# Optimization experiments

Hardware: AMD Instinct MI355X
Metric: run time of the kernel (lower is better)

Reference implementation:

```python
import jax, jax.numpy as jnp
import numpy as np

B, C, H, W = 16, 32, 32, 2048


def setup_inputs() -> dict:
    key = jax.random.key(0)
    ks = jax.random.split(key, 7)
    s = 1.0 / np.sqrt(C * H)  # torch conv2d default init scale (fan_in = C*H*1)
    x = jax.random.normal(ks[0], (B, C, H, W), dtype=jnp.float32)
    wq = jax.random.uniform(ks[1], (C, C, H), jnp.float32, -s, s)
    bq = jax.random.uniform(ks[2], (C,), jnp.float32, -s, s)
    wk = jax.random.uniform(ks[3], (C, C, H), jnp.float32, -s, s)
    bk = jax.random.uniform(ks[4], (C,), jnp.float32, -s, s)
    wv = jax.random.uniform(ks[5], (C, C, H), jnp.float32, -s, s)
    bv = jax.random.uniform(ks[6], (C,), jnp.float32, -s, s)
    return {"x": x, "wq": wq, "bq": bq, "wk": wk, "bk": bk, "wv": wv, "bv": bv}


def _proj(x, w, b):
    # Conv2d kernel (H,1) with no padding == contract over (in_channels, H).
    # x: [B,C,H,W], w: [Cout,Cin,H] -> [B,Cout,W]
    return jnp.einsum('bihw,oih->bow', x, w) + b[None, :, None]


def reference(x, wq, bq, wk, bk, wv, bv):
    q = _proj(x, wq, bq)            # [B,C,W]
    k = _proj(x, wk, bk)            # [B,C,W]
    v = _proj(x, wv, bv)            # [B,C,W]
    # query.permute(0,2,1) @ key -> [B,W,W]; NOTE: unscaled, as in source.
    scores = jnp.einsum('bcw,bcv->bwv', q, k)
    attn = jax.nn.softmax(scores, axis=-1)
    # value @ attention^T -> [B,C,W]
    out = jnp.einsum('bcv,bwv->bcw', v, attn)
    # bilinear upsample (1,W)->(H,W), align_corners=False: width is identity,
    # height replicates the single row -> pure broadcast. Then residual add.
    return out[:, :, None, :] + x
```

## Files before the change

kernel.cpp:

```cpp
#include <hip/hip_runtime.h>
#include <hip/hip_bf16.h>

typedef __bf16 bf16x8 __attribute__((ext_vector_type(8)));
typedef float  f32x4  __attribute__((ext_vector_type(4)));
typedef float  f32x16 __attribute__((ext_vector_type(16)));

#define NB 16
#define NC 32
#define NH 32
#define NW 2048
#define NK (NC*NH)
#define LOG2E 1.4426950408889634f
#define KP 40

static __device__ __forceinline__ unsigned int pk2(float a, float b) {
    union { __bf16 h[2]; unsigned int u; } z;
    z.h[0] = (__bf16)a; z.h[1] = (__bf16)b;
    return z.u;
}

__global__ __launch_bounds__(256) void wprep_kernel(
    const float* __restrict__ wq, const float* __restrict__ wk,
    const float* __restrict__ wv, __bf16* __restrict__ wb)
{
    const int i = blockIdx.x * 256 + threadIdx.x;
    const float* srcs[3] = { wq, wk, wv };
    float4 v = *(const float4*)(srcs[i >> 13] + (size_t)(i & 8191) * 4);
    const float sc = (i >> 13) == 0 ? LOG2E : 1.0f;
    union { __bf16 h[4]; unsigned long long u; } z;
    z.h[0] = (__bf16)(v.x * sc); z.h[1] = (__bf16)(v.y * sc);
    z.h[2] = (__bf16)(v.z * sc); z.h[3] = (__bf16)(v.w * sc);
    *(unsigned long long*)(wb + (size_t)i * 4) = z.u;
}

__global__ __launch_bounds__(384) void proj_kernel(
    const float* __restrict__ x, const __bf16* __restrict__ wb,
    const float* __restrict__ bq, const float* __restrict__ bk,
    const float* __restrict__ bv,
    __bf16* __restrict__ qT, __bf16* __restrict__ kT, __bf16* __restrict__ V)
{
    const int b    = blockIdx.x >> 6;
    const int wt   = blockIdx.x & 63;
    const int nt   = threadIdx.x >> 6;
    const int lane = threadIdx.x & 63;
    const int g    = lane >> 4;
    const int lr   = lane & 15;
    const int w0   = wt * 32;

    __shared__ __bf16 tile[2][32][KP];

    const float* xb = x + (size_t)b * NK * NW;

    const int skr = threadIdx.x >> 3;
    const int swc = (threadIdx.x & 7) * 4;
    const bool stager = (threadIdx.x < 256);
    const float* xs = xb + w0 + swc;

    const __bf16* wrow = wb + (size_t)(nt >> 1) * 32768
                            + (size_t)((nt & 1) * 16 + lr) * NK;

    f32x4 acc0 = {0.f,0.f,0.f,0.f}, acc1 = {0.f,0.f,0.f,0.f};

    f32x4 xv;
    if (stager) {
        xv = *(const f32x4*)(xs + (size_t)skr * NW);
        __bf16* wp = &tile[0][swc][skr];
        wp[0*KP] = (__bf16)xv[0]; wp[1*KP] = (__bf16)xv[1];
        wp[2*KP] = (__bf16)xv[2]; wp[3*KP] = (__bf16)xv[3];
    }
    bf16x8 Bcur = *(const bf16x8*)(wrow + g*8);
    __syncthreads();

    for (int s = 0; s < 32; ++s) {
        const int cur = s & 1;
        f32x4 xn;
        if (s < 31 && stager)
            xn = *(const f32x4*)(xs + (size_t)((s+1)*32 + skr) * NW);
        bf16x8 Bnext;
        if (s < 31)
            Bnext = *(const bf16x8*)(wrow + (s+1)*32 + g*8);

        const bf16x8 af0 = *(const bf16x8*)&tile[cur][lr][g*8];
        const bf16x8 af1 = *(const bf16x8*)&tile[cur][16 + lr][g*8];
        acc0 = __builtin_amdgcn_mfma_f32_16x16x32_bf16(af0, Bcur, acc0, 0, 0, 0);
        acc1 = __builtin_amdgcn_mfma_f32_16x16x32_bf16(af1, Bcur, acc1, 0, 0, 0);

        if (s < 31 && stager) {
            __bf16* wp = &tile[cur ^ 1][swc][skr];
            wp[0*KP] = (__bf16)xn[0]; wp[1*KP] = (__bf16)xn[1];
            wp[2*KP] = (__bf16)xn[2]; wp[3*KP] = (__bf16)xn[3];
        }
        Bcur = Bnext;
        __syncthreads();
    }

    const int pid = nt >> 1;
    const int o   = (nt & 1) * 16 + lr;
    const float* biases[3] = { bq, bk, bv };
    float bb = biases[pid][o];
    if (pid == 0) bb *= LOG2E;

    if (pid < 2) {
        __bf16* dst = (pid ? kT : qT) + (size_t)b * NW * NC;
        #pragma unroll
        for (int r = 0; r < 4; ++r) {
            dst[(size_t)(w0 +      g*4 + r) * NC + o] = (__bf16)(acc0[r] + bb);
            dst[(size_t)(w0 + 16 + g*4 + r) * NC + o] = (__bf16)(acc1[r] + bb);
        }
    } else {
        __bf16* dst = V + ((size_t)b * NC + o) * NW + w0;
        union { __bf16 h[4]; unsigned long long u; } z0, z1;
        #pragma unroll
        for (int r = 0; r < 4; ++r) {
            z0.h[r] = (__bf16)(acc0[r] + bb);
            z1.h[r] = (__bf16)(acc1[r] + bb);
        }
        *(unsigned long long*)(dst +      g*4) = z0.u;
        *(unsigned long long*)(dst + 16 + g*4) = z1.u;
    }
}

__global__ __launch_bounds__(256) void attn_kernel(
    const float* __restrict__ x,
    const __bf16* __restrict__ qT, const __bf16* __restrict__ kT,
    const __bf16* __restrict__ V,
    float* __restrict__ out)
{
    const int b    = blockIdx.x >> 6;
    const int wt   = blockIdx.x & 63;
    const int w0   = wt * 32;
    const int wave = threadIdx.x >> 6;
    const int lane = threadIdx.x & 63;
    const int wl = lane & 31, hi = lane >> 5;
    const int swl = (wl & 0x13) | ((wl & 4) << 1) | ((wl & 8) >> 1);

    const __bf16* qTb = qT + (size_t)b * NW * NC;
    const __bf16* kTb = kT + (size_t)b * NW * NC;
    const __bf16* Vb  = V  + (size_t)b * NC * NW;

    const __bf16* qrow = qTb + (size_t)(w0 + wl) * NC;
    const bf16x8 qf0 = *(const bf16x8*)(qrow + hi*8);
    const bf16x8 qf1 = *(const bf16x8*)(qrow + 16 + hi*8);

    f32x16 acc, z16;
    #pragma unroll
    for (int r = 0; r < 16; ++r) { acc[r] = 0.f; z16[r] = 0.f; }
    float lsum = 0.f;

    const int vbeg = wave * 512;
    const __bf16* kbase = kTb + (size_t)swl * NC;
    const __bf16* vbase = Vb + (size_t)wl * NW;

#define KLD0(V0) (*(const bf16x8*)(kbase + (size_t)(V0) * NC + hi*8))
#define KLD1(V0) (*(const bf16x8*)(kbase + (size_t)(V0) * NC + 16 + hi*8))
#define VLD0(V0) (*(const bf16x8*)(vbase + (V0) + hi*8))
#define VLD1(V0) (*(const bf16x8*)(vbase + (V0) + 16 + hi*8))

    bf16x8 k0r = KLD0(vbeg), k1r = KLD1(vbeg);
    f32x16 s_cur = __builtin_amdgcn_mfma_f32_32x32x16_bf16(k0r, qf0, z16, 0, 0, 0);
    s_cur = __builtin_amdgcn_mfma_f32_32x32x16_bf16(k1r, qf1, s_cur, 0, 0, 0);
    k0r = KLD0(vbeg + 32); k1r = KLD1(vbeg + 32);
    bf16x8 v0r = VLD0(vbeg), v1r = VLD1(vbeg);

    #pragma unroll
    for (int it = 0; it < 16; ++it) {
        f32x16 s_next;
        if (it < 15) {
            s_next = __builtin_amdgcn_mfma_f32_32x32x16_bf16(k0r, qf0, z16, 0, 0, 0);
            s_next = __builtin_amdgcn_mfma_f32_32x32x16_bf16(k1r, qf1, s_next, 0, 0, 0);
        }
        if (it < 14) {
            const int vn = vbeg + (it + 2) * 32;
            k0r = KLD0(vn); k1r = KLD1(vn);
        }

        float p[16];
        #pragma unroll
        for (int r = 0; r < 16; ++r) p[r] = __builtin_amdgcn_exp2f(s_cur[r]);
        float ts[8];
        #pragma unroll
        for (int r = 0; r < 8; ++r) ts[r] = p[r] + p[r+8];
        #pragma unroll
        for (int r = 0; r < 4; ++r) ts[r] += ts[r+4];
        lsum += (ts[0] + ts[1]) + (ts[2] + ts[3]);

        union { unsigned int u[4]; bf16x8 v; } pfa, pfb;
        #pragma unroll
        for (int i = 0; i < 4; ++i) pfa.u[i] = pk2(p[2*i],     p[2*i + 1]);
        #pragma unroll
        for (int i = 0; i < 4; ++i) pfb.u[i] = pk2(p[8 + 2*i], p[8 + 2*i + 1]);

        acc = __builtin_amdgcn_mfma_f32_32x32x16_bf16(v0r, pfa.v, acc, 0, 0, 0);
        acc = __builtin_amdgcn_mfma_f32_32x32x16_bf16(v1r, pfb.v, acc, 0, 0, 0);

        if (it < 15) {
            const int vn = vbeg + (it + 1) * 32;
            v0r = VLD0(vn); v1r = VLD1(vn);
            s_cur = s_next;
        }
    }
#undef KLD0
#undef KLD1
#undef VLD0
#undef VLD1
    lsum += __shfl_xor(lsum, 32);

    __shared__ float sl[4][32];
    __shared__ float sO[4][32][33];
    __shared__ float Of[32][33];

    if (hi == 0) sl[wave][wl] = lsum;
    #pragma unroll
    for (int r = 0; r < 16; ++r) {
        const int c = (r & 3) + 8*(r >> 2) + 4*hi;
        sO[wave][c][wl] = acc[r];
    }
    __syncthreads();

    {
        const int w  = threadIdx.x & 31;
        const int cg = threadIdx.x >> 5;
        const float L = (sl[0][w] + sl[1][w]) + (sl[2][w] + sl[3][w]);
        const float rL = 1.0f / L;
        #pragma unroll
        for (int cc = 0; cc < 4; ++cc) {
            const int c = cg * 4 + cc;
            const float o = ((sO[0][c][w] + sO[1][c][w]) +
                             (sO[2][c][w] + sO[3][c][w]));
            Of[c][w] = o * rL;
        }
    }
    __syncthreads();

    const float* xb = x   + (size_t)b * NC * NH * NW + w0;
    float*       ob = out + (size_t)b * NC * NH * NW + w0;
    const int chunk = threadIdx.x & 7;
    #pragma unroll
    for (int it = 0; it < 32; ++it) {
        const int row = it*32 + (threadIdx.x >> 3);
        const int c = row >> 5, h = row & 31;
        const size_t off = ((size_t)c * NH + h) * NW + chunk*4;
        const f32x4 xv = *(const f32x4*)(xb + off);
        f32x4 ov;
        ov[0] = Of[c][chunk*4 + 0] + xv[0];
        ov[1] = Of[c][chunk*4 + 1] + xv[1];
        ov[2] = Of[c][chunk*4 + 2] + xv[2];
        ov[3] = Of[c][chunk*4 + 3] + xv[3];
        __builtin_nontemporal_store(ov, (f32x4*)(ob + off));
    }
}

extern "C" void kernel_launch(void* const* d_in, const int* in_sizes, int n_in,
                              void* d_out, int out_size, void* d_ws, size_t ws_size,
                              hipStream_t stream)
{
    const float* x  = (const float*)d_in[0];
    const float* wq = (const float*)d_in[1];
    const float* bq = (const float*)d_in[2];
    const float* wk = (const float*)d_in[3];
    const float* bk = (const float*)d_in[4];
    const float* wv = (const float*)d_in[5];
    const float* bv = (const float*)d_in[6];
    float* out = (float*)d_out;

    char* ws = (char*)d_ws;
    __bf16* qT = (__bf16*)(ws);
    __bf16* kT = (__bf16*)(ws + (2u << 20));
    __bf16* V  = (__bf16*)(ws + (4u << 20));
    __bf16* wb = (__bf16*)(ws + (6u << 20));

    hipLaunchKernelGGL(wprep_kernel, dim3(96), dim3(256), 0, stream, wq, wk, wv, wb);
    hipLaunchKernelGGL(proj_kernel, dim3(NB * 64), dim3(384), 0, stream,
                       x, wb, bq, bk, bv, qT, kT, V);
    hipLaunchKernelGGL(attn_kernel, dim3(NB * 64), dim3(256), 0, stream,
                       x, qT, kT, V, out);
}
```

Measured before the change: 93.92 us.

## Split projection into bf16 transpose pass and split-K MFMA projection kernel

Adds a kernel that converts x to bf16 and transposes it to [B,W,K], then a projection kernel where four waves each handle a quarter of K and reduce partials through shared memory. The goal is to remove the in-loop LDS transpose staging from the projection and give it contiguous bf16 loads. The cost is an extra full pass over x (read fp32, write a 64 MB bf16 copy) and an extra launch. The new path runs only if the workspace is at least 72 MB; otherwise it falls back to the old kernel.

```diff
diff --git a/kernel.cpp b/kernel.cpp
--- a/kernel.cpp
+++ b/kernel.cpp
@@ -33,7 +33,126 @@
     *(unsigned long long*)(wb + (size_t)i * 4) = z.u;
 }
 
-__global__ __launch_bounds__(384) void proj_kernel(
+__global__ __launch_bounds__(256) void xtrans_kernel(
+    const float* __restrict__ x, __bf16* __restrict__ xT)
+{
+    const int b  = blockIdx.x >> 8;
+    const int kt = (blockIdx.x >> 4) & 15;
+    const int wt = blockIdx.x & 15;
+    const int k0 = kt * 64, w0 = wt * 128;
+    __shared__ unsigned int tile[128][36];
+
+    const float* xb = x + ((size_t)b * NK + k0) * NW + w0;
+    #pragma unroll
+    for (int i = 0; i < 4; ++i) {
+        const int flat = i * 256 + threadIdx.x;
+        const int kp = flat >> 5;
+        const int wq = flat & 31;
+        const float4 a = *(const float4*)(xb + (size_t)(2*kp)   * NW + wq*4);
+        const float4 c = *(const float4*)(xb + (size_t)(2*kp+1) * NW + wq*4);
+        tile[wq*4+0][kp] = pk2(a.x, c.x);
+        tile[wq*4+1][kp] = pk2(a.y, c.y);
+        tile[wq*4+2][kp] = pk2(a.z, c.z);
+        tile[wq*4+3][kp] = pk2(a.w, c.w);
+    }
+    __syncthreads();
+    __bf16* dst = xT + ((size_t)b * NW + w0) * NK + k0;
+    #pragma unroll
+    for (int i = 0; i < 4; ++i) {
+        const int flat = i * 256 + threadIdx.x;
+        const int w = flat >> 3, c4 = flat & 7;
+        uint4 v;
+        v.x = tile[w][c4*4+0]; v.y = tile[w][c4*4+1];
+        v.z = tile[w][c4*4+2]; v.w = tile[w][c4*4+3];
+        *(uint4*)(dst + (size_t)w * NK + c4*8) = v;
+    }
+}
+
+__global__ __launch_bounds__(256) void projlite_kernel(
+    const __bf16* __restrict__ xT, const __bf16* __restrict__ wb,
+    const float* __restrict__ bq, const float* __restrict__ bk,
+    const float* __restrict__ bv,
+    __bf16* __restrict__ qT, __bf16* __restrict__ kT, __bf16* __restrict__ V)
+{
+    const int b    = blockIdx.x >> 6;
+    const int wt   = blockIdx.x & 63;
+    const int wave = threadIdx.x >> 6;
+    const int lane = threadIdx.x & 63;
+    const int g    = lane >> 4;
+    const int lr   = lane & 15;
+    const int w0   = wt * 32;
+
+    const __bf16* xTb = xT + (size_t)b * NW * NK;
+    const int k0 = wave * 256;
+
+    f32x4 acc[2][6];
+    #pragma unroll
+    for (int mt = 0; mt < 2; ++mt)
+        #pragma unroll
+        for (int nt = 0; nt < 6; ++nt)
+            acc[mt][nt] = f32x4{0.f, 0.f, 0.f, 0.f};
+
+    #pragma unroll
+    for (int ki = 0; ki < 8; ++ki) {
+        const int kk = k0 + ki * 32;
+        bf16x8 af[2];
+        #pragma unroll
+        for (int mt = 0; mt < 2; ++mt)
+            af[mt] = *(const bf16x8*)(xTb + (size_t)(w0 + mt*16 + lr) * NK + kk + g*8);
+        bf16x8 bfv[6];
+        #pragma unroll
+        for (int nt = 0; nt < 6; ++nt)
+            bfv[nt] = *(const bf16x8*)(wb + (size_t)(nt >> 1) * 32768
+                                          + (size_t)((nt & 1) * 16 + lr) * NK
+                                          + kk + g*8);
+        #pragma unroll
+        for (int mt = 0; mt < 2; ++mt)
+            #pragma unroll
+            for (int nt = 0; nt < 6; ++nt)
+                acc[mt][nt] = __builtin_amdgcn_mfma_f32_16x16x32_bf16(
+                    af[mt], bfv[nt], acc[mt][nt], 0, 0, 0);
+    }
+
+    __shared__ f32x4 part[4][12][64];
+    #pragma unroll
+    for (int mt = 0; mt < 2; ++mt)
+        #pragma unroll
+        for (int nt = 0; nt < 6; ++nt)
+            part[wave][mt*6 + nt][lane] = acc[mt][nt];
+    __syncthreads();
+
+    const int mt     = wave & 1;
+    const int ntbase = (wave >> 1) * 3;
+    const float* biases[3] = { bq, bk, bv };
+    #pragma unroll
+    for (int nti = 0; nti < 3; ++nti) {
+        const int nt = ntbase + nti;
+        const int fi = mt*6 + nt;
+        f32x4 s = part[0][fi][lane];
+        #pragma unroll
+        for (int sl = 1; sl < 4; ++sl) s += part[sl][fi][lane];
+        const int pid = nt >> 1;
+        const int o   = (nt & 1) * 16 + lr;
+        float bb = biases[pid][o];
+        if (pid == 0) bb *= LOG2E;
+        if (pid < 2) {
+            __bf16* dst = (pid ? kT : qT) + (size_t)b * NW * NC;
+            #pragma unroll
+            for (int r = 0; r < 4; ++r) {
+                const int w = w0 + mt*16 + g*4 + r;
+                dst[(size_t)w * NC + o] = (__bf16)(s[r] + bb);
+            }
+        } else {
+            union { __bf16 h[4]; unsigned long long u; } z;
+            #pragma unroll
+            for (int r = 0; r < 4; ++r) z.h[r] = (__bf16)(s[r] + bb);
+            __bf16* dst = V + ((size_t)b * NC + o) * NW + (w0 + mt*16 + g*4);
+            *(unsigned long long*)dst = z.u;
+        }
+    }
+}
+
+__global__ __launch_bounds__(384) void projfb_kernel(
     const float* __restrict__ x, const __bf16* __restrict__ wb,
     const float* __restrict__ bq, const float* __restrict__ bk,
     const float* __restrict__ bv,
@@ -50,7 +169,6 @@
     __shared__ __bf16 tile[2][32][KP];
 
     const float* xb = x + (size_t)b * NK * NW;
-
     const int skr = threadIdx.x >> 3;
     const int swc = (threadIdx.x & 7) * 4;
     const bool stager = (threadIdx.x < 256);
@@ -268,10 +386,17 @@
     __bf16* kT = (__bf16*)(ws + (2u << 20));
     __bf16* V  = (__bf16*)(ws + (4u << 20));
     __bf16* wb = (__bf16*)(ws + (6u << 20));
+    __bf16* xT = (__bf16*)(ws + (8u << 20));
 
     hipLaunchKernelGGL(wprep_kernel, dim3(96), dim3(256), 0, stream, wq, wk, wv, wb);
-    hipLaunchKernelGGL(proj_kernel, dim3(NB * 64), dim3(384), 0, stream,
-                       x, wb, bq, bk, bv, qT, kT, V);
+    if (ws_size >= (size_t)(72u << 20)) {
+        hipLaunchKernelGGL(xtrans_kernel, dim3(NB * 256), dim3(256), 0, stream, x, xT);
+        hipLaunchKernelGGL(projlite_kernel, dim3(NB * 64), dim3(256), 0, stream,
+                           xT, wb, bq, bk, bv, qT, kT, V);
+    } else {
+        hipLaunchKernelGGL(projfb_kernel, dim3(NB * 64), dim3(384), 0, stream,
+                           x, wb, bq, bk, bv, qT, kT, V);
+    }
     hipLaunchKernelGGL(attn_kernel, dim3(NB * 64), dim3(256), 0, stream,
                        x, qT, kT, V, out);
 }
```

Result: slower. 128.0 us (+36.3%).

## Split residual broadcast-add epilogue into separate streaming kernel; unroll projection loop

Applied to the files above, without the earlier changes.

The attention kernel no longer streams x and writes the full output. It writes the normalized attention result O [B,C,W] to workspace, and a new epi_kernel reads O once per (b,c,half-row) and adds it to 32 rows of x with contiguous row-wise accesses. This is meant to get better coalescing and memory parallelism for the dominant read-x/write-out traffic, and to keep the attention kernel lighter. The cost is an extra launch plus a small O round trip through memory. The projection k-loop is also fully unrolled.

```diff
diff --git a/kernel.cpp b/kernel.cpp
--- a/kernel.cpp
+++ b/kernel.cpp
@@ -50,7 +50,6 @@
     __shared__ __bf16 tile[2][32][KP];
 
     const float* xb = x + (size_t)b * NK * NW;
-
     const int skr = threadIdx.x >> 3;
     const int swc = (threadIdx.x & 7) * 4;
     const bool stager = (threadIdx.x < 256);
@@ -71,6 +70,7 @@
     bf16x8 Bcur = *(const bf16x8*)(wrow + g*8);
     __syncthreads();
 
+    #pragma unroll
     for (int s = 0; s < 32; ++s) {
         const int cur = s & 1;
         f32x4 xn;
@@ -121,10 +121,9 @@
 }
 
 __global__ __launch_bounds__(256) void attn_kernel(
-    const float* __restrict__ x,
     const __bf16* __restrict__ qT, const __bf16* __restrict__ kT,
     const __bf16* __restrict__ V,
-    float* __restrict__ out)
+    float* __restrict__ O)
 {
     const int b    = blockIdx.x >> 6;
     const int wt   = blockIdx.x & 63;
@@ -207,7 +206,6 @@
 
     __shared__ float sl[4][32];
     __shared__ float sO[4][32][33];
-    __shared__ float Of[32][33];
 
     if (hi == 0) sl[wave][wl] = lsum;
     #pragma unroll
@@ -227,26 +225,34 @@
             const int c = cg * 4 + cc;
             const float o = ((sO[0][c][w] + sO[1][c][w]) +
                              (sO[2][c][w] + sO[3][c][w]));
-            Of[c][w] = o * rL;
-        }
-    }
-    __syncthreads();
-
-    const float* xb = x   + (size_t)b * NC * NH * NW + w0;
-    float*       ob = out + (size_t)b * NC * NH * NW + w0;
-    const int chunk = threadIdx.x & 7;
-    #pragma unroll
-    for (int it = 0; it < 32; ++it) {
-        const int row = it*32 + (threadIdx.x >> 3);
-        const int c = row >> 5, h = row & 31;
-        const size_t off = ((size_t)c * NH + h) * NW + chunk*4;
-        const f32x4 xv = *(const f32x4*)(xb + off);
+            O[((size_t)b * NC + c) * NW + w0 + w] = o * rL;
+        }
+    }
+}
+
+__global__ __launch_bounds__(256) void epi_kernel(
+    const float* __restrict__ x, const float* __restrict__ O,
+    float* __restrict__ out)
+{
+    const int b    = blockIdx.x >> 6;
+    const int c    = (blockIdx.x >> 1) & 31;
+    const int half = blockIdx.x & 1;
+    const int w0   = half * 1024 + threadIdx.x * 4;
+
+    const f32x4 o4 = *(const f32x4*)(O + ((size_t)b * NC + c) * NW + w0);
+    const float* xp = x   + (((size_t)b * NC + c) * NH) * NW + w0;
+    float*       op = out + (((size_t)b * NC + c) * NH) * NW + w0;
+
+    #pragma unroll 8
+    for (int h = 0; h < NH; ++h) {
+        const size_t off = (size_t)h * NW;
+        const f32x4 xv = *(const f32x4*)(xp + off);
         f32x4 ov;
-        ov[0] = Of[c][chunk*4 + 0] + xv[0];
-        ov[1] = Of[c][chunk*4 + 1] + xv[1];
-        ov[2] = Of[c][chunk*4 + 2] + xv[2];
-        ov[3] = Of[c][chunk*4 + 3] + xv[3];
-        __builtin_nontemporal_store(ov, (f32x4*)(ob + off));
+        ov[0] = o4[0] + xv[0];
+        ov[1] = o4[1] + xv[1];
+        ov[2] = o4[2] + xv[2];
+        ov[3] = o4[3] + xv[3];
+        __builtin_nontemporal_store(ov, (f32x4*)(op + off));
     }
 }
 
@@ -268,10 +274,13 @@
     __bf16* kT = (__bf16*)(ws + (2u << 20));
     __bf16* V  = (__bf16*)(ws + (4u << 20));
     __bf16* wb = (__bf16*)(ws + (6u << 20));
+    float*  O  = (float*)(ws + (8u << 20));
 
     hipLaunchKernelGGL(wprep_kernel, dim3(96), dim3(256), 0, stream, wq, wk, wv, wb);
     hipLaunchKernelGGL(proj_kernel, dim3(NB * 64), dim3(384), 0, stream,
                        x, wb, bq, bk, bv, qT, kT, V);
     hipLaunchKernelGGL(attn_kernel, dim3(NB * 64), dim3(256), 0, stream,
-                       x, qT, kT, V, out);
-}
+                       qT, kT, V, O);
+    hipLaunchKernelGGL(epi_kernel, dim3(NB * 64), dim3(256), 0, stream,
+                       x, O, out);
+}
```

New measurement: 104.1 us. 10.8% more time.
